# Kernel optimization log

Measured on AMD Instinct MI355X. Metric: run time of the kernel, lower is better.

The kernel has to match this reference:

```python
import jax, jax.numpy as jnp
import numpy as np

N_NODES = 50000
EPS = 1e-5


def gcn_conv(x, edge_index, edge_weight, W, b, n):
    # PyG GCNConv: h = x @ W; out[dst] += norm * h[src]; out += b
    # with self-loops (weight 1) and symmetric normalization D^-1/2 A D^-1/2.
    src, dst = edge_index[0], edge_index[1]
    loop = jnp.arange(n)
    src_all = jnp.concatenate([src, loop])            # [E+N]
    dst_all = jnp.concatenate([dst, loop])
    w_all = jnp.concatenate([edge_weight, jnp.ones((n,), x.dtype)])
    deg = jax.ops.segment_sum(w_all, dst_all, num_segments=n)
    dinv = jnp.where(deg > 0, jax.lax.rsqrt(jnp.maximum(deg, 1e-30)), 0.0)
    norm = dinv[src_all] * w_all * dinv[dst_all]      # [E+N]
    h = x @ W                                         # [N, out]
    msg = h[src_all] * norm[:, None]                  # [E+N, out]
    return jax.ops.segment_sum(msg, dst_all, num_segments=n) + b


def setup_inputs() -> dict:
    key = jax.random.key(0)
    ks = jax.random.split(key, 8)
    nfeat, nhid, nout = 1024, 256, 256
    E = 800000
    x = jax.random.normal(ks[0], (N_NODES, nfeat), dtype=jnp.float32)
    edge_index = jax.random.randint(ks[1], (2, E), 0, N_NODES, dtype=jnp.int64)
    edge_weight = jax.random.uniform(ks[2], (E,), dtype=jnp.float32)
    W1 = jax.random.normal(ks[3], (nfeat, nhid), dtype=jnp.float32) / np.sqrt(nfeat)
    b1 = jnp.zeros((nhid,), jnp.float32)
    W2 = jax.random.normal(ks[4], (nhid, nout), dtype=jnp.float32) / np.sqrt(nhid)
    b2 = jnp.zeros((nout,), jnp.float32)
    bn_gamma = jnp.ones((nout,), jnp.float32)
    bn_beta = jnp.zeros((nout,), jnp.float32)
    ln_gamma = jnp.ones((nout,), jnp.float32)
    ln_beta = jnp.zeros((nout,), jnp.float32)
    return {"x": x, "edge_index": edge_index, "edge_weight": edge_weight,
            "W1": W1, "b1": b1, "W2": W2, "b2": b2,
            "bn_gamma": bn_gamma, "bn_beta": bn_beta,
            "ln_gamma": ln_gamma, "ln_beta": ln_beta}


def reference(x, edge_index, edge_weight, W1, b1, W2, b2,
              bn_gamma, bn_beta, ln_gamma, ln_beta):
    n = x.shape[0]
    # dropout is identity in eval mode
    h = jax.nn.relu(gcn_conv(x, edge_index, edge_weight, W1, b1, n))
    h = jax.nn.relu(gcn_conv(h, edge_index, edge_weight, W2, b2, n))
    # BatchNorm1d (training-mode batch statistics, biased variance)
    mu = jnp.mean(h, axis=0)
    var = jnp.mean((h - mu) ** 2, axis=0)
    h = (h - mu) * jax.lax.rsqrt(var + EPS) * bn_gamma + bn_beta
    # LayerNorm over feature dim
    lmu = jnp.mean(h, axis=-1, keepdims=True)
    lvar = jnp.mean((h - lmu) ** 2, axis=-1, keepdims=True)
    return (h - lmu) * jax.lax.rsqrt(lvar + EPS) * ln_gamma + ln_beta
```

## Files before the change

### kernel.cpp

```cpp
#include <hip/hip_runtime.h>


typedef __attribute__((ext_vector_type(4))) float f32x4;
typedef __attribute__((ext_vector_type(8))) _Float16 f16x8;
typedef __attribute__((ext_vector_type(4))) _Float16 f16x4;

#define NN 50000
#define NF 1024
#define NH 256

__global__ __launch_bounds__(256) void deg_count(const int* __restrict__ ei,
    const float* __restrict__ ew, float* __restrict__ deg, int* __restrict__ cnt, int E)
{
    int e = blockIdx.x * 256 + threadIdx.x;
    if (e >= E) return;
    int d = ei[E + e];
    atomicAdd(&deg[d], ew[e]);
    atomicAdd(&cnt[d], 1);
}

__global__ __launch_bounds__(256) void dinv_k(const float* __restrict__ deg,
    float* __restrict__ dinv, int n)
{
    int i = blockIdx.x * 256 + threadIdx.x;
    if (i < n) dinv[i] = rsqrtf(deg[i] + 1.0f);
}

__global__ __launch_bounds__(512) void scan_a(const int* __restrict__ cnt,
    int* __restrict__ excl, int* __restrict__ bsum, int n)
{
    __shared__ int sm[512];
    int t = threadIdx.x, g = blockIdx.x * 512 + t;
    int v = (g < n) ? cnt[g] : 0;
    sm[t] = v;
    __syncthreads();
    for (int d = 1; d < 512; d <<= 1) {
        int x = (t >= d) ? sm[t - d] : 0;
        __syncthreads();
        sm[t] += x;
        __syncthreads();
    }
    if (g < n) excl[g] = sm[t] - v;
    if (t == 511) bsum[blockIdx.x] = sm[511];
}

__global__ __launch_bounds__(128) void scan_b(int* __restrict__ bsum, int nb)
{
    __shared__ int sm[128];
    int t = threadIdx.x;
    int v = (t < nb) ? bsum[t] : 0;
    sm[t] = v;
    __syncthreads();
    for (int d = 1; d < 128; d <<= 1) {
        int x = (t >= d) ? sm[t - d] : 0;
        __syncthreads();
        sm[t] += x;
        __syncthreads();
    }
    if (t < nb) bsum[t] = sm[t] - v;
}

__global__ __launch_bounds__(256) void scan_c(const int* __restrict__ excl,
    const int* __restrict__ bsum, int* __restrict__ offs, int n, int E)
{
    int g = blockIdx.x * 256 + threadIdx.x;
    if (g < n) offs[g] = excl[g] + bsum[g >> 9];
    else if (g == n) offs[n] = E;
}

__global__ __launch_bounds__(256) void scatter_k(const int* __restrict__ ei,
    const float* __restrict__ ew, const int* __restrict__ offs,
    int* __restrict__ cursor, const float* __restrict__ dinv,
    int* __restrict__ csrc, float* __restrict__ cwv, int E)
{
    int e = blockIdx.x * 256 + threadIdx.x;
    if (e >= E) return;
    int s = ei[e], d = ei[E + e];
    int pos = offs[d] + atomicAdd(&cursor[d], 1);
    csrc[pos] = s;
    cwv[pos] = ew[e] * dinv[s] * dinv[d];
}

__global__ __launch_bounds__(256) void cvt_w(const float* __restrict__ W,
    unsigned short* __restrict__ WT, int K, int total)
{
    int idx = blockIdx.x * 256 + threadIdx.x;
    if (idx >= total) return;
    int k = idx >> 8, n = idx & 255;
    ((_Float16*)WT)[(size_t)n * K + k] = (_Float16)W[idx];
}

template<bool AF32>
__global__ __launch_bounds__(256) void gemm_mfma(
    const void* __restrict__ Av, const unsigned short* __restrict__ BT,
    _Float16* __restrict__ C, int M, int K)
{
    constexpr int AS = AF32 ? 40 : 32;
    __shared__ _Float16 As[2][128 * AS];
    __shared__ _Float16 Bs[2][128 * 32];
    const int t = threadIdx.x;
    const int lane = t & 63, wid = t >> 6;
    const int r = lane & 15, q = lane >> 4;
    const int n0 = blockIdx.x * 128;
    const int m0 = blockIdx.y * 128;
    const int wm = (wid >> 1) * 64, wn = (wid & 1) * 64;
    const float* Af = (const float*)Av;
    const _Float16* Ah = (const _Float16*)Av;

    f32x4 acc[4][4];
#pragma unroll
    for (int i = 0; i < 4; ++i)
#pragma unroll
        for (int j = 0; j < 4; ++j) acc[i][j] = (f32x4){0.f, 0.f, 0.f, 0.f};

    const int T = K >> 5;
    float4 a_pre[4];

    if constexpr (AF32) {
#pragma unroll
        for (int it = 0; it < 4; ++it) {
            int f = it * 256 + t;
            int m = f >> 3, kc = (f & 7) << 2;
            int gm = m0 + m; if (gm >= M) gm = M - 1;
            a_pre[it] = *(const float4*)(Af + (size_t)gm * K + kc);
        }
    } else {
#pragma unroll
        for (int rd = 0; rd < 2; ++rd) {
            int row = rd * 64 + (t >> 2), kc = (t & 3) << 3;
            int gm = m0 + row; if (gm >= M) gm = M - 1;
            const _Float16* g = Ah + (size_t)gm * K + kc;
            _Float16* l = &As[0][0] + rd * 2048 + wid * 512;
            __builtin_amdgcn_global_load_lds(
                (const __attribute__((address_space(1))) unsigned int*)g,
                (__attribute__((address_space(3))) unsigned int*)l, 16, 0, 0);
        }
    }
#pragma unroll
    for (int rd = 0; rd < 2; ++rd) {
        int c = rd * 256 + t;
        int n = c >> 2, kc = (c & 3) << 3;
        const _Float16* g = (const _Float16*)BT + (size_t)(n0 + n) * K + kc;
        _Float16* l = &Bs[0][0] + rd * 2048 + wid * 512;
        __builtin_amdgcn_global_load_lds(
            (const __attribute__((address_space(1))) unsigned int*)g,
            (__attribute__((address_space(3))) unsigned int*)l, 16, 0, 0);
    }

    for (int k = 0; k < T; ++k) {
        const int cur = k & 1, nxt = cur ^ 1;
        if constexpr (AF32) {
#pragma unroll
            for (int it = 0; it < 4; ++it) {
                int f = it * 256 + t;
                int m = f >> 3, kc = (f & 7) << 2;
                f16x4 hv;
                hv.x = (_Float16)a_pre[it].x; hv.y = (_Float16)a_pre[it].y;
                hv.z = (_Float16)a_pre[it].z; hv.w = (_Float16)a_pre[it].w;
                *(f16x4*)(&As[cur][0] + m * AS + kc) = hv;
            }
        }
        __syncthreads();

        if (k + 1 < T) {
            const int k1 = (k + 1) << 5;
#pragma unroll
            for (int rd = 0; rd < 2; ++rd) {
                int c = rd * 256 + t;
                int n = c >> 2, kc = (c & 3) << 3;
                const _Float16* g = (const _Float16*)BT + (size_t)(n0 + n) * K + k1 + kc;
                _Float16* l = &Bs[nxt][0] + rd * 2048 + wid * 512;
                __builtin_amdgcn_global_load_lds(
                    (const __attribute__((address_space(1))) unsigned int*)g,
                    (__attribute__((address_space(3))) unsigned int*)l, 16, 0, 0);
            }
            if constexpr (AF32) {
#pragma unroll
                for (int it = 0; it < 4; ++it) {
                    int f = it * 256 + t;
                    int m = f >> 3, kc = (f & 7) << 2;
                    int gm = m0 + m; if (gm >= M) gm = M - 1;
                    a_pre[it] = *(const float4*)(Af + (size_t)gm * K + k1 + kc);
                }
            } else {
#pragma unroll
                for (int rd = 0; rd < 2; ++rd) {
                    int row = rd * 64 + (t >> 2), kc = (t & 3) << 3;
                    int gm = m0 + row; if (gm >= M) gm = M - 1;
                    const _Float16* g = Ah + (size_t)gm * K + k1 + kc;
                    _Float16* l = &As[nxt][0] + rd * 2048 + wid * 512;
                    __builtin_amdgcn_global_load_lds(
                        (const __attribute__((address_space(1))) unsigned int*)g,
                        (__attribute__((address_space(3))) unsigned int*)l, 16, 0, 0);
                }
            }
        }

        f16x8 af[4], bfr[4];
#pragma unroll
        for (int i = 0; i < 4; ++i)
            af[i] = *(const f16x8*)(&As[cur][0] + (wm + i * 16 + r) * AS + q * 8);
#pragma unroll
        for (int j = 0; j < 4; ++j)
            bfr[j] = *(const f16x8*)(&Bs[cur][0] + (wn + j * 16 + r) * 32 + q * 8);
#pragma unroll
        for (int i = 0; i < 4; ++i)
#pragma unroll
            for (int j = 0; j < 4; ++j)
                acc[i][j] = __builtin_amdgcn_mfma_f32_16x16x32_f16(af[i], bfr[j], acc[i][j], 0, 0, 0);
    }

#pragma unroll
    for (int i = 0; i < 4; ++i) {
#pragma unroll
        for (int reg = 0; reg < 4; ++reg) {
            int m = m0 + wm + i * 16 + q * 4 + reg;
            if (m < M) {
                _Float16* cp = C + (size_t)m * 256 + (n0 + wn + r);
#pragma unroll
                for (int j = 0; j < 4; ++j) cp[j * 16] = (_Float16)acc[i][j][reg];
            }
        }
    }
}

__global__ __launch_bounds__(256) void agg_relu(
    const _Float16* __restrict__ h, const int* __restrict__ roff,
    const int* __restrict__ csrc, const float* __restrict__ cwv,
    const float* __restrict__ dinv, const float* __restrict__ bias,
    _Float16* __restrict__ out, int n)
{
    const int lane = threadIdx.x & 63, wid = threadIdx.x >> 6;
    const int i = blockIdx.x * 4 + wid;
    if (i >= n) return;
    const int c = lane << 2;
    const float di = dinv[i];
    const float sw = di * di;
    const f16x4 hv = *(const f16x4*)(h + (size_t)i * 256 + c);
    float a0 = sw * (float)hv.x, a1 = sw * (float)hv.y;
    float a2 = sw * (float)hv.z, a3 = sw * (float)hv.w;
    float c0 = 0.f, c1 = 0.f, c2 = 0.f, c3 = 0.f;
    const int p0 = roff[i], pe = roff[i + 1];
    for (int base = p0; base < pe; base += 64) {
        int lim = pe - base; if (lim > 64) lim = 64;
        int sv = 0; float wv = 0.f;
        if (lane < lim) { sv = csrc[base + lane]; wv = cwv[base + lane]; }
        int j = 0;
        for (; j + 1 < lim; j += 2) {
            int s0 = __shfl(sv, j), s1 = __shfl(sv, j + 1);
            float w0 = __shfl(wv, j), w1 = __shfl(wv, j + 1);
            f16x4 v0 = *(const f16x4*)(h + (size_t)s0 * 256 + c);
            f16x4 v1 = *(const f16x4*)(h + (size_t)s1 * 256 + c);
            a0 += w0 * (float)v0.x; a1 += w0 * (float)v0.y;
            a2 += w0 * (float)v0.z; a3 += w0 * (float)v0.w;
            c0 += w1 * (float)v1.x; c1 += w1 * (float)v1.y;
            c2 += w1 * (float)v1.z; c3 += w1 * (float)v1.w;
        }
        if (j < lim) {
            int s0 = __shfl(sv, j);
            float w0 = __shfl(wv, j);
            f16x4 v0 = *(const f16x4*)(h + (size_t)s0 * 256 + c);
            a0 += w0 * (float)v0.x; a1 += w0 * (float)v0.y;
            a2 += w0 * (float)v0.z; a3 += w0 * (float)v0.w;
        }
    }
    const float4 bb = *(const float4*)(bias + c);
    f16x4 o;
    o.x = (_Float16)fmaxf(a0 + c0 + bb.x, 0.f);
    o.y = (_Float16)fmaxf(a1 + c1 + bb.y, 0.f);
    o.z = (_Float16)fmaxf(a2 + c2 + bb.z, 0.f);
    o.w = (_Float16)fmaxf(a3 + c3 + bb.w, 0.f);
    *(f16x4*)(out + (size_t)i * 256 + c) = o;
}

__global__ __launch_bounds__(256) void bn_stats(const _Float16* __restrict__ h,
    float* __restrict__ bnsum, float* __restrict__ bnsq, int n)
{
    const int t = threadIdx.x;
    float s = 0.f, s2 = 0.f;
    for (int r = blockIdx.x; r < n; r += gridDim.x) {
        float v = (float)h[(size_t)r * 256 + t];
        s += v; s2 += v * v;
    }
    atomicAdd(&bnsum[t], s);
    atomicAdd(&bnsq[t], s2);
}

__global__ __launch_bounds__(256) void bn_params(const float* __restrict__ bnsum,
    const float* __restrict__ bnsq, const float* __restrict__ gamma,
    const float* __restrict__ beta, float* __restrict__ scale,
    float* __restrict__ shift, int n)
{
    int t = threadIdx.x;
    float mu = bnsum[t] / (float)n;
    float var = bnsq[t] / (float)n - mu * mu;
    float sc = gamma[t] * rsqrtf(var + 1e-5f);
    scale[t] = sc;
    shift[t] = beta[t] - mu * sc;
}

__global__ __launch_bounds__(256) void bn_ln(const _Float16* __restrict__ h,
    const float* __restrict__ scale, const float* __restrict__ shift,
    const float* __restrict__ lng, const float* __restrict__ lnb,
    float* __restrict__ out, int n)
{
    const int lane = threadIdx.x & 63, wid = threadIdx.x >> 6;
    const int i = blockIdx.x * 4 + wid;
    if (i >= n) return;
    const int c = lane << 2;
    const f16x4 v = *(const f16x4*)(h + (size_t)i * 256 + c);
    const float4 sc = *(const float4*)(scale + c);
    const float4 sh = *(const float4*)(shift + c);
    float y0 = (float)v.x * sc.x + sh.x;
    float y1 = (float)v.y * sc.y + sh.y;
    float y2 = (float)v.z * sc.z + sh.z;
    float y3 = (float)v.w * sc.w + sh.w;
    float ps = y0 + y1 + y2 + y3;
    float ps2 = y0 * y0 + y1 * y1 + y2 * y2 + y3 * y3;
#pragma unroll
    for (int off = 32; off > 0; off >>= 1) {
        ps += __shfl_down(ps, off);
        ps2 += __shfl_down(ps2, off);
    }
    ps = __shfl(ps, 0);
    ps2 = __shfl(ps2, 0);
    const float mu = ps * (1.f / 256.f);
    const float var = ps2 * (1.f / 256.f) - mu * mu;
    const float rs = rsqrtf(var + 1e-5f);
    const float4 g = *(const float4*)(lng + c);
    const float4 bb = *(const float4*)(lnb + c);
    float4 o;
    o.x = (y0 - mu) * rs * g.x + bb.x;
    o.y = (y1 - mu) * rs * g.y + bb.y;
    o.z = (y2 - mu) * rs * g.z + bb.z;
    o.w = (y3 - mu) * rs * g.w + bb.w;
    *(float4*)(out + (size_t)i * 256 + c) = o;
}

extern "C" void kernel_launch(void* const* d_in, const int* in_sizes, int n_in,
                              void* d_out, int out_size, void* d_ws, size_t ws_size,
                              hipStream_t stream)
{
    const float* x   = (const float*)d_in[0];
    const int*   ei  = (const int*)d_in[1];
    const float* ew  = (const float*)d_in[2];
    const float* W1  = (const float*)d_in[3];
    const float* b1  = (const float*)d_in[4];
    const float* W2  = (const float*)d_in[5];
    const float* b2  = (const float*)d_in[6];
    const float* bng = (const float*)d_in[7];
    const float* bnb = (const float*)d_in[8];
    const float* lng = (const float*)d_in[9];
    const float* lnb = (const float*)d_in[10];
    float* out = (float*)d_out;

    const int N = NN;
    const int E = in_sizes[2];

    char* ws = (char*)d_ws;
    size_t o = 0;
    auto alloc = [&](size_t b) -> char* {
        char* p = ws + o;
        o = (o + b + 255) & ~(size_t)255;
        return p;
    };
    _Float16* h1  = (_Float16*)alloc((size_t)N * NH * 2);
    _Float16* h1a = (_Float16*)alloc((size_t)N * NH * 2);
    _Float16* h2a = (_Float16*)alloc((size_t)N * NH * 2);
    unsigned short* W1T = (unsigned short*)alloc((size_t)NH * NF * 2);
    unsigned short* W2T = (unsigned short*)alloc((size_t)NH * NH * 2);
    int*   csrc = (int*)alloc((size_t)E * 4);
    float* cwv  = (float*)alloc((size_t)E * 4);
    int*   offs = (int*)alloc((size_t)(N + 1) * 4);
    int*   excl = (int*)alloc((size_t)N * 4);
    int*   bsum = (int*)alloc(512);
    float* dinv = (float*)alloc((size_t)N * 4);
    float* bnscale = (float*)alloc(NH * 4);
    float* bnshift = (float*)alloc(NH * 4);
    char* zbase = ws + o;
    float* deg    = (float*)alloc((size_t)N * 4);
    int*   cnt    = (int*)alloc((size_t)N * 4);
    int*   cursor = (int*)alloc((size_t)N * 4);
    float* bnsum  = (float*)alloc(NH * 4);
    float* bnsq   = (float*)alloc(NH * 4);
    size_t zbytes = (size_t)((ws + o) - zbase);
    (void)hipMemsetAsync(zbase, 0, zbytes, stream);

    cvt_w<<<(NF * NH + 255) / 256, 256, 0, stream>>>(W1, W1T, NF, NF * NH);
    cvt_w<<<(NH * NH + 255) / 256, 256, 0, stream>>>(W2, W2T, NH, NH * NH);
    deg_count<<<(E + 255) / 256, 256, 0, stream>>>(ei, ew, deg, cnt, E);
    dinv_k<<<(N + 255) / 256, 256, 0, stream>>>(deg, dinv, N);
    scan_a<<<(N + 511) / 512, 512, 0, stream>>>(cnt, excl, bsum, N);
    scan_b<<<1, 128, 0, stream>>>(bsum, (N + 511) / 512);
    scan_c<<<(N + 1 + 255) / 256, 256, 0, stream>>>(excl, bsum, offs, N, E);
    scatter_k<<<(E + 255) / 256, 256, 0, stream>>>(ei, ew, offs, cursor, dinv, csrc, cwv, E);

    dim3 gg(2, (N + 127) / 128);
    gemm_mfma<true><<<gg, 256, 0, stream>>>(x, W1T, h1, N, NF);
    agg_relu<<<(N + 3) / 4, 256, 0, stream>>>(h1, offs, csrc, cwv, dinv, b1, h1a, N);
    gemm_mfma<false><<<gg, 256, 0, stream>>>(h1a, W2T, h1, N, NH);
    agg_relu<<<(N + 3) / 4, 256, 0, stream>>>(h1, offs, csrc, cwv, dinv, b2, h2a, N);

    bn_stats<<<256, 256, 0, stream>>>(h2a, bnsum, bnsq, N);
    bn_params<<<1, 256, 0, stream>>>(bnsum, bnsq, bng, bnb, bnscale, bnshift, N);
    bn_ln<<<(N + 3) / 4, 256, 0, stream>>>(h2a, bnscale, bnshift, lng, lnb, out, N);
}
```

Measured before the change: 696.7 us.

## Restructure GEMM to load A directly into registers with full-width N tiles

The GEMM is rewritten so each wave loads its 16 rows of A straight from global memory into MFMA fragment registers, skipping the LDS staging of A. Each block now covers all 256 output columns for 64 rows, so x is read exactly once instead of once per column tile. B is double-buffered in LDS, A is prefetched two steps ahead, waits use explicit vmcnt, and launch bounds request 3 blocks per CU. The aim is to cut redundant reads of the large fp32 input and LDS traffic, at the cost of less B reuse per block and tricky hand-written wait counts that could introduce races.

```diff
diff --git a/kernel.cpp b/kernel.cpp
--- a/kernel.cpp
+++ b/kernel.cpp
@@ -91,135 +91,101 @@
 }
 
 template<bool AF32>
-__global__ __launch_bounds__(256) void gemm_mfma(
+__global__ __launch_bounds__(256, 3) void gemm_direct(
     const void* __restrict__ Av, const unsigned short* __restrict__ BT,
     _Float16* __restrict__ C, int M, int K)
 {
-    constexpr int AS = AF32 ? 40 : 32;
-    __shared__ _Float16 As[2][128 * AS];
-    __shared__ _Float16 Bs[2][128 * 32];
+    __shared__ _Float16 Bs[2][256 * 32];
     const int t = threadIdx.x;
     const int lane = t & 63, wid = t >> 6;
     const int r = lane & 15, q = lane >> 4;
-    const int n0 = blockIdx.x * 128;
-    const int m0 = blockIdx.y * 128;
-    const int wm = (wid >> 1) * 64, wn = (wid & 1) * 64;
+    const int m0 = blockIdx.x * 64;
     const float* Af = (const float*)Av;
     const _Float16* Ah = (const _Float16*)Av;
 
-    f32x4 acc[4][4];
-#pragma unroll
-    for (int i = 0; i < 4; ++i)
-#pragma unroll
-        for (int j = 0; j < 4; ++j) acc[i][j] = (f32x4){0.f, 0.f, 0.f, 0.f};
+    int gm = m0 + wid * 16 + r;
+    if (gm >= M) gm = M - 1;
+
+    f32x4 acc[16];
+#pragma unroll
+    for (int j = 0; j < 16; ++j) acc[j] = (f32x4){0.f, 0.f, 0.f, 0.f};
 
     const int T = K >> 5;
-    float4 a_pre[4];
-
-    if constexpr (AF32) {
-#pragma unroll
-        for (int it = 0; it < 4; ++it) {
-            int f = it * 256 + t;
-            int m = f >> 3, kc = (f & 7) << 2;
-            int gm = m0 + m; if (gm >= M) gm = M - 1;
-            a_pre[it] = *(const float4*)(Af + (size_t)gm * K + kc);
-        }
-    } else {
-#pragma unroll
-        for (int rd = 0; rd < 2; ++rd) {
-            int row = rd * 64 + (t >> 2), kc = (t & 3) << 3;
-            int gm = m0 + row; if (gm >= M) gm = M - 1;
-            const _Float16* g = Ah + (size_t)gm * K + kc;
-            _Float16* l = &As[0][0] + rd * 2048 + wid * 512;
+
+    auto issueB = [&](int kt, int buf) {
+        const int k0 = kt << 5;
+#pragma unroll
+        for (int rd = 0; rd < 4; ++rd) {
+            int n = rd * 64 + wid * 16 + (lane >> 2);
+            int kc = (lane & 3) << 3;
+            const _Float16* g = (const _Float16*)BT + (size_t)n * K + k0 + kc;
+            _Float16* l = &Bs[buf][0] + rd * 2048 + wid * 512;
             __builtin_amdgcn_global_load_lds(
                 (const __attribute__((address_space(1))) unsigned int*)g,
                 (__attribute__((address_space(3))) unsigned int*)l, 16, 0, 0);
         }
-    }
-#pragma unroll
-    for (int rd = 0; rd < 2; ++rd) {
-        int c = rd * 256 + t;
-        int n = c >> 2, kc = (c & 3) << 3;
-        const _Float16* g = (const _Float16*)BT + (size_t)(n0 + n) * K + kc;
-        _Float16* l = &Bs[0][0] + rd * 2048 + wid * 512;
-        __builtin_amdgcn_global_load_lds(
-            (const __attribute__((address_space(1))) unsigned int*)g,
-            (__attribute__((address_space(3))) unsigned int*)l, 16, 0, 0);
-    }
+    };
+
+    f32x4 apf[2][2];
+    f16x8 aph[2];
+
+    auto issueA = [&](int kt, int slot) {
+        if constexpr (AF32) {
+            const float* g = Af + (size_t)gm * K + (kt << 5) + q * 8;
+            apf[slot][0] = *(const f32x4*)g;
+            apf[slot][1] = *(const f32x4*)(g + 4);
+        } else {
+            aph[slot] = *(const f16x8*)(Ah + (size_t)gm * K + (kt << 5) + q * 8);
+        }
+    };
+
+    issueB(0, 0);
+    issueA(0, 0);
+    issueB(1, 1);
+    issueA(1, 1);
 
     for (int k = 0; k < T; ++k) {
-        const int cur = k & 1, nxt = cur ^ 1;
+        const int cur = k & 1;
+
+        f16x8 af;
         if constexpr (AF32) {
 #pragma unroll
-            for (int it = 0; it < 4; ++it) {
-                int f = it * 256 + t;
-                int m = f >> 3, kc = (f & 7) << 2;
-                f16x4 hv;
-                hv.x = (_Float16)a_pre[it].x; hv.y = (_Float16)a_pre[it].y;
-                hv.z = (_Float16)a_pre[it].z; hv.w = (_Float16)a_pre[it].w;
-                *(f16x4*)(&As[cur][0] + m * AS + kc) = hv;
+            for (int e = 0; e < 4; ++e) {
+                af[e]     = (_Float16)apf[cur][0][e];
+                af[4 + e] = (_Float16)apf[cur][1][e];
             }
-        }
-        __syncthreads();
-
-        if (k + 1 < T) {
-            const int k1 = (k + 1) << 5;
-#pragma unroll
-            for (int rd = 0; rd < 2; ++rd) {
-                int c = rd * 256 + t;
-                int n = c >> 2, kc = (c & 3) << 3;
-                const _Float16* g = (const _Float16*)BT + (size_t)(n0 + n) * K + k1 + kc;
-                _Float16* l = &Bs[nxt][0] + rd * 2048 + wid * 512;
-                __builtin_amdgcn_global_load_lds(
-                    (const __attribute__((address_space(1))) unsigned int*)g,
-                    (__attribute__((address_space(3))) unsigned int*)l, 16, 0, 0);
-            }
-            if constexpr (AF32) {
-#pragma unroll
-                for (int it = 0; it < 4; ++it) {
-                    int f = it * 256 + t;
-                    int m = f >> 3, kc = (f & 7) << 2;
-                    int gm = m0 + m; if (gm >= M) gm = M - 1;
-                    a_pre[it] = *(const float4*)(Af + (size_t)gm * K + k1 + kc);
-                }
-            } else {
-#pragma unroll
-                for (int rd = 0; rd < 2; ++rd) {
-                    int row = rd * 64 + (t >> 2), kc = (t & 3) << 3;
-                    int gm = m0 + row; if (gm >= M) gm = M - 1;
-                    const _Float16* g = Ah + (size_t)gm * K + k1 + kc;
-                    _Float16* l = &As[nxt][0] + rd * 2048 + wid * 512;
-                    __builtin_amdgcn_global_load_lds(
-                        (const __attribute__((address_space(1))) unsigned int*)g,
-                        (__attribute__((address_space(3))) unsigned int*)l, 16, 0, 0);
-                }
-            }
-        }
-
-        f16x8 af[4], bfr[4];
-#pragma unroll
-        for (int i = 0; i < 4; ++i)
-            af[i] = *(const f16x8*)(&As[cur][0] + (wm + i * 16 + r) * AS + q * 8);
-#pragma unroll
-        for (int j = 0; j < 4; ++j)
-            bfr[j] = *(const f16x8*)(&Bs[cur][0] + (wn + j * 16 + r) * 32 + q * 8);
-#pragma unroll
-        for (int i = 0; i < 4; ++i)
-#pragma unroll
-            for (int j = 0; j < 4; ++j)
-                acc[i][j] = __builtin_amdgcn_mfma_f32_16x16x32_f16(af[i], bfr[j], acc[i][j], 0, 0, 0);
-    }
-
-#pragma unroll
-    for (int i = 0; i < 4; ++i) {
-#pragma unroll
-        for (int reg = 0; reg < 4; ++reg) {
-            int m = m0 + wm + i * 16 + q * 4 + reg;
-            if (m < M) {
-                _Float16* cp = C + (size_t)m * 256 + (n0 + wn + r);
-#pragma unroll
-                for (int j = 0; j < 4; ++j) cp[j * 16] = (_Float16)acc[i][j][reg];
-            }
+        } else {
+            af = aph[cur];
+        }
+
+        if (k < T - 1) {
+            if constexpr (AF32) asm volatile("s_waitcnt vmcnt(2)" ::: "memory");
+            else                asm volatile("s_waitcnt vmcnt(1)" ::: "memory");
+        } else {
+            asm volatile("s_waitcnt vmcnt(0)" ::: "memory");
+        }
+        __builtin_amdgcn_s_barrier();
+        __builtin_amdgcn_sched_barrier(0);
+
+        if (k >= 1 && k + 1 < T) issueB(k + 1, cur ^ 1);
+        __builtin_amdgcn_sched_barrier(0);
+        if (k + 2 < T) issueA(k + 2, cur);
+        __builtin_amdgcn_sched_barrier(0);
+
+#pragma unroll
+        for (int j = 0; j < 16; ++j) {
+            f16x8 bfr = *(const f16x8*)(&Bs[cur][0] + (j * 16 + r) * 32 + q * 8);
+            acc[j] = __builtin_amdgcn_mfma_f32_16x16x32_f16(af, bfr, acc[j], 0, 0, 0);
+        }
+    }
+
+#pragma unroll
+    for (int reg = 0; reg < 4; ++reg) {
+        int m = m0 + wid * 16 + q * 4 + reg;
+        if (m < M) {
+            _Float16* cp = C + (size_t)m * 256 + r;
+#pragma unroll
+            for (int j = 0; j < 16; ++j) cp[j * 16] = (_Float16)acc[j][reg];
         }
     }
 }
@@ -395,10 +361,10 @@
     scan_c<<<(N + 1 + 255) / 256, 256, 0, stream>>>(excl, bsum, offs, N, E);
     scatter_k<<<(E + 255) / 256, 256, 0, stream>>>(ei, ew, offs, cursor, dinv, csrc, cwv, E);
 
-    dim3 gg(2, (N + 127) / 128);
-    gemm_mfma<true><<<gg, 256, 0, stream>>>(x, W1T, h1, N, NF);
+    const int gblk = (N + 63) / 64;
+    gemm_direct<true><<<gblk, 256, 0, stream>>>(x, W1T, h1, N, NF);
     agg_relu<<<(N + 3) / 4, 256, 0, stream>>>(h1, offs, csrc, cwv, dinv, b1, h1a, N);
-    gemm_mfma<false><<<gg, 256, 0, stream>>>(h1a, W2T, h1, N, NH);
+    gemm_direct<false><<<gblk, 256, 0, stream>>>(h1a, W2T, h1, N, NH);
     agg_relu<<<(N + 3) / 4, 256, 0, stream>>>(h1, offs, csrc, cwv, dinv, b2, h2a, N);
 
     bn_stats<<<256, 256, 0, stream>>>(h2a, bnsum, bnsq, N);
```

Measured after the change: 739.5 us. 1.06x slower.
